# Optimization experiments

Measured on AMD Instinct MI355X. Metric: run time of the kernel, lower is better.

## Reference

```python
import jax, jax.numpy as jnp
import numpy as np

E = 512      # embed_size
H = 1024     # hidden_size
HH = H // 2  # per-direction encoder hidden
VS = 32000   # src vocab
VT = 32000   # tgt vocab
B = 32
S = 48       # src len
T = 48       # tgt decode steps (tgt_tokens has T+1 tokens incl <s>, </s>)


def setup_inputs() -> dict:
    key = jax.random.key(0)
    ks = jax.random.split(key, 24)
    rn = lambda k, shape: (jax.random.normal(k, shape) * 0.05).astype(jnp.float32)

    src_lengths = jax.random.randint(ks[0], (B,), S // 2, S + 1)
    src_tokens = jax.random.randint(ks[1], (B, S), 3, VS)
    src_tokens = jnp.where(jnp.arange(S)[None, :] < src_lengths[:, None], src_tokens, 0)
    tgt_lengths = jax.random.randint(ks[2], (B,), T // 2, T + 1)
    tgt_tokens = jax.random.randint(ks[3], (B, T + 1), 3, VT)
    tgt_tokens = jnp.where(jnp.arange(T + 1)[None, :] <= tgt_lengths[:, None], tgt_tokens, 0)

    return dict(
        enc_embed=rn(ks[4], (VS, E)),
        dec_embed=rn(ks[5], (VT, E)),
        enc_Wih_f=rn(ks[6], (4 * HH, E)), enc_Whh_f=rn(ks[7], (4 * HH, HH)),
        enc_bih_f=rn(ks[8], (4 * HH,)),   enc_bhh_f=rn(ks[9], (4 * HH,)),
        enc_Wih_b=rn(ks[10], (4 * HH, E)), enc_Whh_b=rn(ks[11], (4 * HH, HH)),
        enc_bih_b=rn(ks[12], (4 * HH,)),   enc_bhh_b=rn(ks[13], (4 * HH,)),
        dec_Wih=rn(ks[14], (4 * H, E + H)), dec_Whh=rn(ks[15], (4 * H, H)),
        dec_bih=rn(ks[16], (4 * H,)),       dec_bhh=rn(ks[17], (4 * H,)),
        Ws_W=rn(ks[18], (VT, 2 * H)), Ws_b=rn(ks[19], (VT,)),
        src_tokens=src_tokens, src_lengths=src_lengths, tgt_tokens=tgt_tokens,
    )


def _lstm_cell(x, h, c, Wih, Whh, bih, bhh):
    # torch gate order: i, f, g, o
    gates = x @ Wih.T + bih + h @ Whh.T + bhh
    i, f, g, o = jnp.split(gates, 4, axis=-1)
    c_new = jax.nn.sigmoid(f) * c + jax.nn.sigmoid(i) * jnp.tanh(g)
    h_new = jax.nn.sigmoid(o) * jnp.tanh(c_new)
    return h_new, c_new


def _masked_lstm(x, mask, Wih, Whh, bih, bhh, hid):
    # x: [B,S,Din], mask: [B,S] bool. Emulates packed LSTM: state frozen and
    # output zero at padded steps.
    Bn = x.shape[0]
    h0 = jnp.zeros((Bn, hid), x.dtype)
    c0 = jnp.zeros((Bn, hid), x.dtype)

    def step(carry, inp):
        h, c = carry
        xt, mt = inp  # [B,Din], [B]
        hn, cn = _lstm_cell(xt, h, c, Wih, Whh, bih, bhh)
        m = mt[:, None]
        h = jnp.where(m, hn, h)
        c = jnp.where(m, cn, c)
        return (h, c), h * m

    (hT, cT), outs = jax.lax.scan(step, (h0, c0), (jnp.swapaxes(x, 0, 1), mask.T))
    return jnp.swapaxes(outs, 0, 1), hT, cT  # [B,S,hid]


def reference(enc_embed, dec_embed,
              enc_Wih_f, enc_Whh_f, enc_bih_f, enc_bhh_f,
              enc_Wih_b, enc_Whh_b, enc_bih_b, enc_bhh_b,
              dec_Wih, dec_Whh, dec_bih, dec_bhh,
              Ws_W, Ws_b,
              src_tokens, src_lengths, tgt_tokens):
    src_mask = jnp.arange(S)[None, :] < src_lengths[:, None]  # [B,S]

    # ---- encoder (bi-LSTM over packed sequence) ----
    emb = enc_embed[src_tokens]  # [B,S,E]
    out_f, hf, _ = _masked_lstm(emb, src_mask, enc_Wih_f, enc_Whh_f, enc_bih_f, enc_bhh_f, HH)
    # backward direction: reverse each sequence within its own length
    rev_idx = jnp.clip(src_lengths[:, None] - 1 - jnp.arange(S)[None, :], 0)  # [B,S]
    emb_rev = jnp.take_along_axis(emb, rev_idx[:, :, None], axis=1)
    out_r, hb, _ = _masked_lstm(emb_rev, src_mask, enc_Wih_b, enc_Whh_b, enc_bih_b, enc_bhh_b, HH)
    out_b = jnp.take_along_axis(out_r, rev_idx[:, :, None], axis=1) * src_mask[:, :, None]
    src_enc = jnp.concatenate([out_f, out_b], axis=-1)  # [B,S,H]
    h0 = jnp.concatenate([hf, hb], axis=-1)  # [B,H]  (h.transpose(0,1).reshape)
    c0 = jnp.zeros_like(h0)
    # NOTE: the torch code reshapes the final LSTM c state the same way; replicate:
    # we need final c from both directions
    # (recompute via _masked_lstm returning c)
    _, _, cf = _masked_lstm(emb, src_mask, enc_Wih_f, enc_Whh_f, enc_bih_f, enc_bhh_f, HH)
    _, _, cb = _masked_lstm(emb_rev, src_mask, enc_Wih_b, enc_Whh_b, enc_bih_b, enc_bhh_b, HH)
    c0 = jnp.concatenate([cf, cb], axis=-1)

    # ---- decoder: per-step LSTM + bmm attention ----
    tgt_in = tgt_tokens[:, :-1]   # [B,T]
    target = tgt_tokens[:, 1:]    # [B,T]
    dec_emb = dec_embed[tgt_in]   # [B,T,E]
    fmask = src_mask.astype(src_enc.dtype)

    def dstep(carry, emb_t):
        h, c, wa = carry  # wa: previous attention context [B,H]
        x = jnp.concatenate([wa, emb_t], axis=-1)  # cat((context, embed)) as in torch
        h, c = _lstm_cell(x, h, c, dec_Wih, dec_Whh, dec_bih, dec_bhh)
        align = jnp.einsum('bsh,bh->bs', src_enc, h)          # bmm scores
        a = jax.nn.softmax(align, axis=1) * fmask              # softmax then mask
        a = a / jnp.sum(a, axis=1, keepdims=True)              # renormalize
        wa = jnp.einsum('bsh,bs->bh', src_enc, a)              # weighted average
        out_t = jnp.concatenate([wa, h], axis=-1)              # [B,2H]
        return (h, c, wa), out_t

    wa0 = jnp.zeros((tgt_in.shape[0], H), src_enc.dtype)
    _, outs = jax.lax.scan(dstep, (h0, c0, wa0), jnp.swapaxes(dec_emb, 0, 1))
    outs = jnp.swapaxes(outs, 0, 1)  # [B,T,2H]

    logits = jnp.einsum('btd,vd->btv', outs, Ws_W) + Ws_b
    logp = jax.nn.log_softmax(logits, axis=-1)
    nll = -jnp.take_along_axis(logp, target[:, :, None], axis=-1)[:, :, 0]
    valid = (target != 0).astype(nll.dtype)  # ignore_index=0, reduction='sum'
    return jnp.sum(nll * valid)
```

## Files before the change

kernel.cpp:

```cpp
#include <hip/hip_runtime.h>
#include <hip/hip_bf16.h>
#include <math.h>

#define EE   512
#define HJ   1024
#define VV   32000
#define BB   32
#define SS   48
#define TT   48

typedef float f32x4 __attribute__((ext_vector_type(4)));
typedef __bf16 bf16x8 __attribute__((ext_vector_type(8)));
typedef __bf16 bf16x4 __attribute__((ext_vector_type(4)));

__device__ __forceinline__ bf16x8 ld_coh_x8(const __bf16* p) {
  bf16x8 r;
  asm volatile("global_load_dwordx4 %0, %1, off sc0 sc1" : "=v"(r) : "v"(p) : "memory");
  return r;
}
__device__ __forceinline__ void st_coh_b16(__bf16* p, __bf16 v) {
  unsigned int w = __builtin_bit_cast(unsigned short, v);
  asm volatile("global_store_short %0, %1, off sc0 sc1" :: "v"(p), "v"(w) : "memory");
}

__device__ __forceinline__ void gbar(int* flags, int step, int nb) {
  asm volatile("s_waitcnt vmcnt(0)" ::: "memory");
  __syncthreads();
  if (threadIdx.x == 0)
    __hip_atomic_store(flags + blockIdx.x * 16, step, __ATOMIC_RELAXED,
                       __HIP_MEMORY_SCOPE_AGENT);
  if (threadIdx.x < nb)
    while (__hip_atomic_load(flags + threadIdx.x * 16, __ATOMIC_RELAXED,
                             __HIP_MEMORY_SCOPE_AGENT) < step)
      __builtin_amdgcn_s_sleep(1);
  __syncthreads();
}

__global__ void embed_src_kernel(const float* __restrict__ enc_embed,
                                 const int* __restrict__ src_tokens,
                                 const int* __restrict__ src_lengths,
                                 __bf16* __restrict__ emb, __bf16* __restrict__ embR) {
  int idx = blockIdx.x * 256 + threadIdx.x;
  if (idx >= BB * SS * EE) return;
  int e = idx & (EE - 1);
  int bs = idx >> 9;
  int b = bs / SS, s = bs % SS;
  int tok = src_tokens[b * SS + s];
  emb[idx] = (__bf16)enc_embed[(size_t)tok * EE + e];
  int len = src_lengths[b];
  int rs = len - 1 - s; if (rs < 0) rs = 0;
  int tokr = src_tokens[b * SS + rs];
  embR[idx] = (__bf16)enc_embed[(size_t)tokr * EE + e];
}

__global__ void embed_tgt_kernel(const float* __restrict__ dec_embed,
                                 const int* __restrict__ tgt_tokens,
                                 __bf16* __restrict__ demb) {
  int idx = blockIdx.x * 256 + threadIdx.x;
  if (idx >= BB * TT * EE) return;
  int e = idx & (EE - 1);
  int bt = idx >> 9;
  int b = bt / TT, t = bt % TT;
  int tok = tgt_tokens[b * (TT + 1) + t];
  demb[idx] = (__bf16)dec_embed[(size_t)tok * EE + e];
}

__global__ void f2bf_kernel(const float* __restrict__ src, __bf16* __restrict__ dst, int n4) {
  int i = blockIdx.x * 256 + threadIdx.x;
  if (i >= n4) return;
  float4 v = ((const float4*)src)[i];
  bf16x4 p = {(__bf16)v.x, (__bf16)v.y, (__bf16)v.z, (__bf16)v.w};
  ((bf16x4*)dst)[i] = p;
}

__global__ void f2bf_slice_kernel(const float* __restrict__ src, __bf16* __restrict__ dst,
                                  int rows, int cols, int ld, int c0) {
  int idx = blockIdx.x * 256 + threadIdx.x;
  if (idx >= rows * cols) return;
  int r = idx / cols, cc = idx % cols;
  dst[idx] = (__bf16)src[(size_t)r * ld + c0 + cc];
}

__global__ void wdec_build_kernel(const float* __restrict__ dWih, const float* __restrict__ dWhh,
                                  __bf16* __restrict__ Wd) {
  int idx = blockIdx.x * 256 + threadIdx.x;
  if (idx >= 4096 * 2048) return;
  int r = idx >> 11, k = idx & 2047;
  float v = (k < 1024) ? dWih[(size_t)r * 1536 + k] : dWhh[(size_t)r * 1024 + (k - 1024)];
  Wd[idx] = (__bf16)v;
}

__global__ void sencT_build(const __bf16* __restrict__ senc, __bf16* __restrict__ sencT) {
  int b = blockIdx.x >> 4, jt = blockIdx.x & 15;
  int j0c = jt * 64;
  __shared__ __bf16 tile[48][72];
  for (int idx = threadIdx.x; idx < 48 * 64; idx += 256) {
    int s = idx >> 6, j = idx & 63;
    tile[s][j] = senc[((size_t)b * SS + s) * 1024 + j0c + j];
  }
  __syncthreads();
  for (int idx = threadIdx.x; idx < 64 * 48; idx += 256) {
    int j = idx / 48, s = idx - j * 48;
    sencT[((size_t)b * 1024 + j0c + j) * 48 + s] = tile[s][j];
  }
}

__global__ __launch_bounds__(256) void gemm_bf16_kernel(
    const __bf16* __restrict__ A, const __bf16* __restrict__ Bm,
    const float* __restrict__ bias1, const float* __restrict__ bias2,
    float* __restrict__ C, int K, int N) {
  const int m0 = blockIdx.x * 128;
  const int n0 = blockIdx.y * 128;
  __shared__ __bf16 As[128 * 40];
  __shared__ __bf16 Bs[128 * 40];
  const int tid = threadIdx.x;
  const int lane = tid & 63, wave = tid >> 6;
  const int wm = (wave >> 1) * 64, wn = (wave & 1) * 64;
  const f32x4 zero = {0.f, 0.f, 0.f, 0.f};
  f32x4 acc[4][4];
  for (int i = 0; i < 4; i++) for (int j = 0; j < 4; j++) acc[i][j] = zero;
  const int r = tid >> 2, seg = tid & 3;
  const int mr = lane & 15, q8 = (lane >> 4) * 8;
  for (int k0 = 0; k0 < K; k0 += 32) {
    *(float4*)&As[r * 40 + seg * 8]        = *(const float4*)&A[(size_t)(m0 + r) * K + k0 + seg * 8];
    *(float4*)&As[(r + 64) * 40 + seg * 8] = *(const float4*)&A[(size_t)(m0 + r + 64) * K + k0 + seg * 8];
    *(float4*)&Bs[r * 40 + seg * 8]        = *(const float4*)&Bm[(size_t)(n0 + r) * K + k0 + seg * 8];
    *(float4*)&Bs[(r + 64) * 40 + seg * 8] = *(const float4*)&Bm[(size_t)(n0 + r + 64) * K + k0 + seg * 8];
    __syncthreads();
    bf16x8 af[4], bfr[4];
    for (int i = 0; i < 4; i++) af[i]  = *(const bf16x8*)&As[(wm + i * 16 + mr) * 40 + q8];
    for (int i = 0; i < 4; i++) bfr[i] = *(const bf16x8*)&Bs[(wn + i * 16 + mr) * 40 + q8];
    for (int i = 0; i < 4; i++)
      for (int j = 0; j < 4; j++)
        acc[i][j] = __builtin_amdgcn_mfma_f32_16x16x32_bf16(af[i], bfr[j], acc[i][j], 0, 0, 0);
    __syncthreads();
  }
  const int col = lane & 15, q = lane >> 4;
  for (int i = 0; i < 4; i++) {
    int rowg = m0 + wm + i * 16 + q * 4;
    for (int j = 0; j < 4; j++) {
      int cg = n0 + wn + j * 16 + col;
      float bb = bias1[cg] + bias2[cg];
      for (int rr = 0; rr < 4; rr++)
        C[(size_t)(rowg + rr) * N + cg] = acc[i][j][rr] + bb;
    }
  }
}

template <int BF>
__global__ __launch_bounds__(256) void logits_kernel(
    const __bf16* __restrict__ A, const void* __restrict__ Braw,
    const float* __restrict__ Wsb, float* __restrict__ rowsum) {
  const int m0 = blockIdx.x * 128;
  const int n0 = blockIdx.y * 128;
  __shared__ __bf16 As[128 * 40];
  __shared__ __bf16 Bs[128 * 40];
  const int tid = threadIdx.x;
  const int lane = tid & 63, wave = tid >> 6;
  const int wm = (wave >> 1) * 64, wn = (wave & 1) * 64;
  const f32x4 zero = {0.f, 0.f, 0.f, 0.f};
  f32x4 acc[4][4];
  for (int i = 0; i < 4; i++) for (int j = 0; j < 4; j++) acc[i][j] = zero;
  const int r = tid >> 2, seg = tid & 3;
  const int rowb = tid >> 1, koff = (tid & 1) * 16;
  const int mr = lane & 15, q8 = (lane >> 4) * 8;
  for (int k0 = 0; k0 < 2048; k0 += 32) {
    *(float4*)&As[r * 40 + seg * 8]        = *(const float4*)&A[(size_t)(m0 + r) * 2048 + k0 + seg * 8];
    *(float4*)&As[(r + 64) * 40 + seg * 8] = *(const float4*)&A[(size_t)(m0 + r + 64) * 2048 + k0 + seg * 8];
    if (BF) {
      const __bf16* Bb = (const __bf16*)Braw;
      *(float4*)&Bs[r * 40 + seg * 8]        = *(const float4*)&Bb[(size_t)(n0 + r) * 2048 + k0 + seg * 8];
      *(float4*)&Bs[(r + 64) * 40 + seg * 8] = *(const float4*)&Bb[(size_t)(n0 + r + 64) * 2048 + k0 + seg * 8];
    } else {
      const float* gb = (const float*)Braw + (size_t)(n0 + rowb) * 2048 + k0 + koff;
      float4 v0 = *(const float4*)(gb);
      float4 v1 = *(const float4*)(gb + 4);
      float4 v2 = *(const float4*)(gb + 8);
      float4 v3 = *(const float4*)(gb + 12);
      bf16x8 p0 = {(__bf16)v0.x,(__bf16)v0.y,(__bf16)v0.z,(__bf16)v0.w,
                   (__bf16)v1.x,(__bf16)v1.y,(__bf16)v1.z,(__bf16)v1.w};
      bf16x8 p1 = {(__bf16)v2.x,(__bf16)v2.y,(__bf16)v2.z,(__bf16)v2.w,
                   (__bf16)v3.x,(__bf16)v3.y,(__bf16)v3.z,(__bf16)v3.w};
      *(bf16x8*)&Bs[rowb * 40 + koff]     = p0;
      *(bf16x8*)&Bs[rowb * 40 + koff + 8] = p1;
    }
    __syncthreads();
    bf16x8 af[4], bfr[4];
    for (int i = 0; i < 4; i++) af[i]  = *(const bf16x8*)&As[(wm + i * 16 + mr) * 40 + q8];
    for (int i = 0; i < 4; i++) bfr[i] = *(const bf16x8*)&Bs[(wn + i * 16 + mr) * 40 + q8];
    for (int i = 0; i < 4; i++)
      for (int j = 0; j < 4; j++)
        acc[i][j] = __builtin_amdgcn_mfma_f32_16x16x32_bf16(af[i], bfr[j], acc[i][j], 0, 0, 0);
    __syncthreads();
  }
  const int col = lane & 15, q = lane >> 4;
  for (int i = 0; i < 4; i++) {
    float s0 = 0, s1 = 0, s2 = 0, s3 = 0;
    for (int j = 0; j < 4; j++) {
      int cg = n0 + wn + j * 16 + col;
      float bb = Wsb[cg];
      s0 += expf(acc[i][j][0] + bb);
      s1 += expf(acc[i][j][1] + bb);
      s2 += expf(acc[i][j][2] + bb);
      s3 += expf(acc[i][j][3] + bb);
    }
    for (int off = 1; off < 16; off <<= 1) {
      s0 += __shfl_xor(s0, off, 64);
      s1 += __shfl_xor(s1, off, 64);
      s2 += __shfl_xor(s2, off, 64);
      s3 += __shfl_xor(s3, off, 64);
    }
    if (col == 0) {
      int rowg = m0 + wm + i * 16 + q * 4;
      atomicAdd(&rowsum[rowg],     s0);
      atomicAdd(&rowsum[rowg + 1], s1);
      atomicAdd(&rowsum[rowg + 2], s2);
      atomicAdd(&rowsum[rowg + 3], s3);
    }
  }
}

__global__ __launch_bounds__(256) void enc_persistent(
    const __bf16* __restrict__ Wenc,
    const float* __restrict__ xg,
    const int* __restrict__ lens,
    __bf16* __restrict__ g_h,
    float* __restrict__ cenc,
    __bf16* __restrict__ ob,
    int* __restrict__ flags) {
  const int bk = blockIdx.x;
  const int dir = bk >> 7;
  const int u0 = (bk & 127) * 4;
  const int tid = threadIdx.x;
  const int lane = tid & 63, wave = tid >> 6;
  __shared__ __bf16 Wl[16 * 520];
  __shared__ float gsc[4 * 512];
  __shared__ float cl[128], hloc[128];
  {
    int row = tid >> 4, t16 = tid & 15;
    int g = row >> 2, du = row & 3;
    const __bf16* src = Wenc + ((size_t)dir * 2048 + g * 512 + u0 + du) * 512;
    for (int c = t16 * 32, e = t16 * 32 + 32; c < e; c += 8)
      *(bf16x8*)&Wl[row * 520 + c] = *(const bf16x8*)&src[c];
  }
  if (tid < 128) { cl[tid] = 0.f; hloc[tid] = 0.f; }
  __syncthreads();
  __bf16* ghd = g_h + dir * 32768;
  __bf16* obd = ob + (size_t)dir * (1536 * 512);
  const float* xgd = xg + (size_t)dir * 1536 * 2048;
  const int nr = lane & 15, q8 = (lane >> 4) * 8;
  for (int t = 0; t < SS; t++) {
    const int cur = t & 1;
    const __bf16* hc = ghd + cur * 16384;
    __bf16* hnx = ghd + (cur ^ 1) * 16384;
    float xv[4];
    if (tid < 128) {
      int b = tid >> 2, du = tid & 3;
#pragma unroll
      for (int g = 0; g < 4; g++)
        xv[g] = xgd[((size_t)b * SS + t) * 2048 + g * 512 + u0 + du];
    }
    f32x4 acc0 = {0.f,0.f,0.f,0.f}, acc1 = {0.f,0.f,0.f,0.f};
    const int kb = wave * 128;
    bf16x8 a0[4], a1[4];
#pragma unroll
    for (int ks = 0; ks < 4; ks++) {
      int k0 = kb + ks * 32;
      a0[ks] = ld_coh_x8(&hc[nr * 512 + k0 + q8]);
      a1[ks] = ld_coh_x8(&hc[(nr + 16) * 512 + k0 + q8]);
    }
    asm volatile("s_waitcnt vmcnt(0)" ::: "memory");
    __builtin_amdgcn_sched_barrier(0);
#pragma unroll
    for (int ks = 0; ks < 4; ks++) {
      int k0 = kb + ks * 32;
      bf16x8 bf_ = *(const bf16x8*)&Wl[nr * 520 + k0 + q8];
      acc0 = __builtin_amdgcn_mfma_f32_16x16x32_bf16(a0[ks], bf_, acc0, 0, 0, 0);
      acc1 = __builtin_amdgcn_mfma_f32_16x16x32_bf16(a1[ks], bf_, acc1, 0, 0, 0);
    }
#pragma unroll
    for (int rg = 0; rg < 4; rg++) {
      int m = (lane >> 4) * 4 + rg;
      gsc[wave * 512 + m * 16 + nr]       = acc0[rg];
      gsc[wave * 512 + 256 + m * 16 + nr] = acc1[rg];
    }
    __syncthreads();
    if (tid < 128) {
      int b = tid >> 2, du = tid & 3;
      float gt[4];
#pragma unroll
      for (int g = 0; g < 4; g++) {
        int base = (b >> 4) * 256 + (b & 15) * 16 + g * 4 + du;
        gt[g] = xv[g] + gsc[base] + gsc[512 + base] + gsc[1024 + base] + gsc[1536 + base];
      }
      bool m_ = t < lens[b];
      float cold = cl[tid], hold = hloc[tid];
      float si = 1.f / (1.f + __expf(-gt[0])), sf = 1.f / (1.f + __expf(-gt[1]));
      float so = 1.f / (1.f + __expf(-gt[3]));
      float cn = sf * cold + si * tanhf(gt[2]);
      float hv = so * tanhf(cn);
      float cne = m_ ? cn : cold;
      float hne = m_ ? hv : hold;
      cl[tid] = cne; hloc[tid] = hne;
      st_coh_b16(&hnx[b * 512 + u0 + du], (__bf16)hne);
      obd[((size_t)b * SS + t) * 512 + u0 + du] = m_ ? (__bf16)hv : (__bf16)0.f;
    }
    gbar(flags, t + 1, 256);
  }
  if (tid < 128) {
    int b = tid >> 2, du = tid & 3;
    cenc[(size_t)dir * 16384 + b * 512 + u0 + du] = cl[tid];
  }
}

__global__ void compose_kernel(const __bf16* __restrict__ ob, const __bf16* __restrict__ g_h,
                               const float* __restrict__ cenc, const int* __restrict__ lens,
                               __bf16* __restrict__ senc, __bf16* __restrict__ g_x0,
                               float* __restrict__ cdec) {
  int idx = blockIdx.x * 256 + threadIdx.x;
  const int N1 = 1536 * 1024;
  if (idx < N1) {
    int u = idx & 1023, bs = idx >> 10, b = bs / SS, s = bs - b * SS;
    __bf16 v;
    if (u < 512) v = ob[(size_t)bs * 512 + u];
    else {
      int len = lens[b];
      if (s < len) {
        int rs = len - 1 - s;
        v = ob[(size_t)(1536 * 512) + ((size_t)b * SS + rs) * 512 + (u - 512)];
      } else v = (__bf16)0.f;
    }
    senc[idx] = v;
  } else if (idx < N1 + 32 * 2048) {
    int k = idx - N1;
    int b = k >> 11, u = k & 2047;
    __bf16 v = (__bf16)0.f;
    if (u >= 1024) {
      int uu = u - 1024;
      v = (uu < 512) ? g_h[b * 512 + uu] : g_h[32768 + b * 512 + (uu - 512)];
    }
    g_x0[k] = v;
  } else if (idx < N1 + 32 * 2048 + 32 * 1024) {
    int k = idx - N1 - 32 * 2048;
    int b = k >> 10, u = k & 1023;
    cdec[k] = (u < 512) ? cenc[b * 512 + u] : cenc[16384 + b * 512 + (u - 512)];
  }
}

__global__ __launch_bounds__(256) void dec_persistent(
    const __bf16* __restrict__ Wd,
    const float* __restrict__ pre,
    const __bf16* __restrict__ senc,
    const __bf16* __restrict__ sencT,
    const int* __restrict__ lens,
    const float* __restrict__ cdec,
    __bf16* __restrict__ xbuf,
    __bf16* __restrict__ outs,
    int* __restrict__ flags) {
  const int bk = blockIdx.x;
  const int u0 = bk * 8;
  const int tid = threadIdx.x, lane = tid & 63, wave = tid >> 6;
  __shared__ __bf16 Wl[32 * 2056];
  __shared__ float gsc[4 * 1024];
  __shared__ float cl[256];
  __shared__ float asm_l[48];
  {
    int row = tid >> 3, t8 = tid & 7;
    int g = row >> 3, du = row & 7;
    const __bf16* src = Wd + (size_t)(g * 1024 + u0 + du) * 2048;
    for (int c = t8 * 256, e = t8 * 256 + 256; c < e; c += 8)
      *(bf16x8*)&Wl[row * 2056 + c] = *(const bf16x8*)&src[c];
  }
  cl[tid] = cdec[(size_t)(tid >> 3) * 1024 + u0 + (tid & 7)];
  __syncthreads();
  const int nr = lane & 15, q8 = (lane >> 4) * 8;
  const int bC = bk >> 2, j0 = (bk & 3) * 256;
  const int b_ = tid >> 3, du_ = tid & 7;
  float xv[4];
#pragma unroll
  for (int g = 0; g < 4; g++)
    xv[g] = pre[((size_t)b_ * TT) * 4096 + g * 1024 + u0 + du_];
  for (int t = 0; t < TT; t++) {
    const __bf16* xc = xbuf + (size_t)t * 65536;
    __bf16* xn = xbuf + (size_t)(t + 1) * 65536;
    f32x4 acc00 = {0.f,0.f,0.f,0.f}, acc01 = {0.f,0.f,0.f,0.f};
    f32x4 acc10 = {0.f,0.f,0.f,0.f}, acc11 = {0.f,0.f,0.f,0.f};
    const int kb = wave * 512;
    bf16x8 a0[16], a1[16];
    if (wave < 2) {
#pragma unroll
      for (int ks = 0; ks < 16; ks++) {
        int k0 = kb + ks * 32;
        a0[ks] = *(const bf16x8*)&xc[nr * 2048 + k0 + q8];
        a1[ks] = *(const bf16x8*)&xc[(nr + 16) * 2048 + k0 + q8];
      }
    } else {
#pragma unroll
      for (int ks = 0; ks < 16; ks++) {
        int k0 = kb + ks * 32;
        a0[ks] = ld_coh_x8(&xc[nr * 2048 + k0 + q8]);
        a1[ks] = ld_coh_x8(&xc[(nr + 16) * 2048 + k0 + q8]);
      }
      asm volatile("s_waitcnt vmcnt(0)" ::: "memory");
      __builtin_amdgcn_sched_barrier(0);
    }
#pragma unroll
    for (int ks = 0; ks < 16; ks++) {
      int k0 = kb + ks * 32;
      bf16x8 b0 = *(const bf16x8*)&Wl[nr * 2056 + k0 + q8];
      bf16x8 b1 = *(const bf16x8*)&Wl[(nr + 16) * 2056 + k0 + q8];
      acc00 = __builtin_amdgcn_mfma_f32_16x16x32_bf16(a0[ks], b0, acc00, 0, 0, 0);
      acc01 = __builtin_amdgcn_mfma_f32_16x16x32_bf16(a0[ks], b1, acc01, 0, 0, 0);
      acc10 = __builtin_amdgcn_mfma_f32_16x16x32_bf16(a1[ks], b0, acc10, 0, 0, 0);
      acc11 = __builtin_amdgcn_mfma_f32_16x16x32_bf16(a1[ks], b1, acc11, 0, 0, 0);
    }
#pragma unroll
    for (int rg = 0; rg < 4; rg++) {
      int m = (lane >> 4) * 4 + rg;
      gsc[wave * 1024 + m * 32 + nr]             = acc00[rg];
      gsc[wave * 1024 + m * 32 + 16 + nr]        = acc01[rg];
      gsc[wave * 1024 + (16 + m) * 32 + nr]      = acc10[rg];
      gsc[wave * 1024 + (16 + m) * 32 + 16 + nr] = acc11[rg];
    }
    __syncthreads();
    {
      float gt[4];
#pragma unroll
      for (int g = 0; g < 4; g++) {
        int base = b_ * 32 + g * 8 + du_;
        gt[g] = xv[g] + gsc[base] + gsc[1024 + base] + gsc[2048 + base] + gsc[3072 + base];
      }
      float cold = cl[tid];
      float si = 1.f / (1.f + __expf(-gt[0])), sf = 1.f / (1.f + __expf(-gt[1]));
      float so = 1.f / (1.f + __expf(-gt[3]));
      float cn = sf * cold + si * tanhf(gt[2]);
      float hv = so * tanhf(cn);
      cl[tid] = cn;
      __bf16 hb = (__bf16)hv;
      st_coh_b16(&xn[b_ * 2048 + 1024 + u0 + du_], hb);
      outs[((size_t)b_ * TT + t) * 2048 + 1024 + u0 + du_] = hb;
    }
    if (t + 1 < TT) {
#pragma unroll
      for (int g = 0; g < 4; g++)
        xv[g] = pre[((size_t)b_ * TT + t + 1) * 4096 + g * 1024 + u0 + du_];
    }
    gbar(flags, 2 * t + 1, 128);
    {
      int len = lens[bC];
      const __bf16* hh = xn + bC * 2048 + 1024;
      bf16x8 h0 = ld_coh_x8(&hh[lane * 16]);
      bf16x8 h1 = ld_coh_x8(&hh[lane * 16 + 8]);
      asm volatile("s_waitcnt vmcnt(0)" ::: "memory");
      __builtin_amdgcn_sched_barrier(0);
      float hf[16];
#pragma unroll
      for (int i = 0; i < 8; i++) { hf[i] = (float)h0[i]; hf[8 + i] = (float)h1[i]; }
      for (int si = 0; si < 12; si++) {
        int s = wave * 12 + si;
        if (s >= len) { if (lane == 0) asm_l[s] = -1e30f; continue; }
        const __bf16* se = senc + ((size_t)bC * SS + s) * 1024;
        bf16x8 s0 = *(const bf16x8*)&se[lane * 16];
        bf16x8 s1 = *(const bf16x8*)&se[lane * 16 + 8];
        float p = 0.f;
#pragma unroll
        for (int i = 0; i < 8; i++) p += (float)s0[i] * hf[i] + (float)s1[i] * hf[8 + i];
#pragma unroll
        for (int off = 32; off > 0; off >>= 1) p += __shfl_xor(p, off, 64);
        if (lane == 0) asm_l[s] = p;
      }
      __syncthreads();
      if (wave == 0) {
        float a = (lane < SS) ? asm_l[lane] : -1e30f;
        float mx = a;
#pragma unroll
        for (int off = 32; off > 0; off >>= 1) mx = fmaxf(mx, __shfl_xor(mx, off, 64));
        float p = (lane < SS) ? __expf(a - mx) : 0.f;
        float sm = p;
#pragma unroll
        for (int off = 32; off > 0; off >>= 1) sm += __shfl_xor(sm, off, 64);
        if (lane < SS) asm_l[lane] = p / sm;
      }
      __syncthreads();
      {
        int j = j0 + tid;
        const __bf16* srow = sencT + ((size_t)bC * 1024 + j) * 48;
        bf16x8 v0 = *(const bf16x8*)&srow[0];
        bf16x8 v1 = *(const bf16x8*)&srow[8];
        bf16x8 v2 = *(const bf16x8*)&srow[16];
        bf16x8 v3 = *(const bf16x8*)&srow[24];
        bf16x8 v4 = *(const bf16x8*)&srow[32];
        bf16x8 v5 = *(const bf16x8*)&srow[40];
        float w = 0.f;
#pragma unroll
        for (int i = 0; i < 8; i++) {
          w += asm_l[i]      * (float)v0[i];
          w += asm_l[8 + i]  * (float)v1[i];
          w += asm_l[16 + i] * (float)v2[i];
          w += asm_l[24 + i] * (float)v3[i];
          w += asm_l[32 + i] * (float)v4[i];
          w += asm_l[40 + i] * (float)v5[i];
        }
        __bf16 wb = (__bf16)w;
        st_coh_b16(&xn[bC * 2048 + j], wb);
        outs[((size_t)bC * TT + t) * 2048 + j] = wb;
      }
    }
    gbar(flags, 2 * t + 2, 128);
  }
}

__global__ __launch_bounds__(256) void tgt_logit_kernel(
    const __bf16* __restrict__ outs_bf, const float* __restrict__ WsW,
    const float* __restrict__ Wsb, const int* __restrict__ tgt_tokens,
    float* __restrict__ tlogit) {
  const int r = blockIdx.x;
  const int b = r / TT, t = r % TT;
  const int tgt = tgt_tokens[b * (TT + 1) + t + 1];
  const __bf16* a = outs_bf + (size_t)r * 2048;
  const float* w = WsW + (size_t)tgt * 2048;
  const int tid = threadIdx.x;
  float p = 0;
  for (int k = tid; k < 2048; k += 256) p += (float)a[k] * w[k];
  for (int off = 32; off > 0; off >>= 1) p += __shfl_down(p, off, 64);
  __shared__ float red[4];
  if ((tid & 63) == 0) red[tid >> 6] = p;
  __syncthreads();
  if (tid == 0) tlogit[r] = red[0] + red[1] + red[2] + red[3] + Wsb[tgt];
}

__global__ void final_kernel(const float* __restrict__ rowsum, const float* __restrict__ tlogit,
                             const int* __restrict__ tgt_tokens, float* __restrict__ out) {
  const int tid = threadIdx.x;
  float s = 0;
  for (int r = tid; r < BB * TT; r += 256) {
    int b = r / TT, t = r % TT;
    int tgt = tgt_tokens[b * (TT + 1) + t + 1];
    if (tgt != 0) s += logf(rowsum[r]) - tlogit[r];
  }
  for (int off = 32; off > 0; off >>= 1) s += __shfl_down(s, off, 64);
  __shared__ float red[4];
  if ((tid & 63) == 0) red[tid >> 6] = s;
  __syncthreads();
  if (tid == 0) out[0] = red[0] + red[1] + red[2] + red[3];
}

extern "C" void kernel_launch(void* const* d_in, const int* in_sizes, int n_in,
                              void* d_out, int out_size, void* d_ws, size_t ws_size,
                              hipStream_t stream) {
  const float* enc_embed = (const float*)d_in[0];
  const float* dec_embed = (const float*)d_in[1];
  const float* eWih_f = (const float*)d_in[2];
  const float* eWhh_f = (const float*)d_in[3];
  const float* ebih_f = (const float*)d_in[4];
  const float* ebhh_f = (const float*)d_in[5];
  const float* eWih_b = (const float*)d_in[6];
  const float* eWhh_b = (const float*)d_in[7];
  const float* ebih_b = (const float*)d_in[8];
  const float* ebhh_b = (const float*)d_in[9];
  const float* dWih = (const float*)d_in[10];
  const float* dWhh = (const float*)d_in[11];
  const float* dbih = (const float*)d_in[12];
  const float* dbhh = (const float*)d_in[13];
  const float* WsW  = (const float*)d_in[14];
  const float* Wsb  = (const float*)d_in[15];
  const int* src_tokens  = (const int*)d_in[16];
  const int* src_lengths = (const int*)d_in[17];
  const int* tgt_tokens  = (const int*)d_in[18];
  float* W = (float*)d_ws;

  size_t o = 0;
  auto alloc = [&](size_t n) { size_t r = o; o += (n + 63) & ~(size_t)63; return r; };
  const size_t flagsE = alloc(256 * 16);
  const size_t flagsD = alloc(256 * 16);
  const size_t ghenc = alloc(32768);
  const size_t rsum  = alloc(BB * TT);
  const size_t zbytes = o * sizeof(float);
  const size_t cenc  = alloc(2 * BB * 512);
  const size_t cdec  = alloc(BB * 1024);
  const size_t tlog  = alloc(BB * TT);
  const size_t xg    = alloc((size_t)2 * 1536 * 2048);
  const size_t pre   = alloc((size_t)1536 * 4096);
  const size_t obuf  = alloc((size_t)2 * 1536 * 512 / 2);
  const size_t senc  = alloc((size_t)1536 * 1024 / 2);
  const size_t sencT = alloc((size_t)32 * 1024 * 48 / 2);
  const size_t gx    = alloc((size_t)49 * 32 * 2048 / 2);
  const size_t wdec  = alloc((size_t)4096 * 2048 / 2);
  const size_t wenc  = alloc((size_t)2 * 2048 * 512 / 2);
  const size_t embbf = alloc(786432 / 2);
  const size_t embRbf= alloc(786432 / 2);
  const size_t dembbf= alloc(786432 / 2);
  const size_t wihfbf= alloc(1048576 / 2);
  const size_t wihbbf= alloc(1048576 / 2);
  const size_t dwihebf = alloc((size_t)4096 * 512 / 2);
  const size_t outsbf  = alloc((size_t)1536 * 2048 / 2);
  const size_t wsbf    = alloc((size_t)VV * 2048 / 2);
  const bool wsbf_fit  = (o * sizeof(float)) <= ws_size;

  (void)hipMemsetAsync(W, 0, zbytes, stream);

  embed_src_kernel<<<3072, 256, 0, stream>>>(enc_embed, src_tokens, src_lengths,
                                             (__bf16*)(W + embbf), (__bf16*)(W + embRbf));
  embed_tgt_kernel<<<3072, 256, 0, stream>>>(dec_embed, tgt_tokens, (__bf16*)(W + dembbf));
  f2bf_kernel<<<1024, 256, 0, stream>>>(eWih_f, (__bf16*)(W + wihfbf), 262144);
  f2bf_kernel<<<1024, 256, 0, stream>>>(eWih_b, (__bf16*)(W + wihbbf), 262144);
  f2bf_kernel<<<1024, 256, 0, stream>>>(eWhh_f, (__bf16*)(W + wenc), 262144);
  f2bf_kernel<<<1024, 256, 0, stream>>>(eWhh_b, (__bf16*)(W + wenc) + 1048576, 262144);
  f2bf_slice_kernel<<<8192, 256, 0, stream>>>(dWih, (__bf16*)(W + dwihebf), 4096, 512, 1536, 1024);
  wdec_build_kernel<<<32768, 256, 0, stream>>>(dWih, dWhh, (__bf16*)(W + wdec));
  if (wsbf_fit)
    f2bf_kernel<<<64000, 256, 0, stream>>>(WsW, (__bf16*)(W + wsbf), VV * 2048 / 4);

  gemm_bf16_kernel<<<dim3(12, 16), 256, 0, stream>>>((__bf16*)(W + embbf), (__bf16*)(W + wihfbf),
                                                     ebih_f, ebhh_f, W + xg, 512, 2048);
  gemm_bf16_kernel<<<dim3(12, 16), 256, 0, stream>>>((__bf16*)(W + embRbf), (__bf16*)(W + wihbbf),
                                                     ebih_b, ebhh_b, W + xg + (size_t)1536 * 2048, 512, 2048);
  gemm_bf16_kernel<<<dim3(12, 32), 256, 0, stream>>>((__bf16*)(W + dembbf), (__bf16*)(W + dwihebf),
                                                     dbih, dbhh, W + pre, 512, 4096);

  enc_persistent<<<256, 256, 0, stream>>>((__bf16*)(W + wenc), W + xg, src_lengths,
                                          (__bf16*)(W + ghenc), W + cenc,
                                          (__bf16*)(W + obuf), (int*)(W + flagsE));
  compose_kernel<<<6528, 256, 0, stream>>>((__bf16*)(W + obuf), (__bf16*)(W + ghenc),
                                           W + cenc, src_lengths,
                                           (__bf16*)(W + senc), (__bf16*)(W + gx), W + cdec);
  sencT_build<<<512, 256, 0, stream>>>((const __bf16*)(W + senc), (__bf16*)(W + sencT));
  dec_persistent<<<128, 256, 0, stream>>>((__bf16*)(W + wdec), W + pre, (__bf16*)(W + senc),
                                          (const __bf16*)(W + sencT),
                                          src_lengths, W + cdec, (__bf16*)(W + gx),
                                          (__bf16*)(W + outsbf), (int*)(W + flagsD));

  if (wsbf_fit)
    logits_kernel<1><<<dim3(12, 250), 256, 0, stream>>>((const __bf16*)(W + outsbf),
                                                        (const void*)(W + wsbf), Wsb, W + rsum);
  else
    logits_kernel<0><<<dim3(12, 250), 256, 0, stream>>>((const __bf16*)(W + outsbf),
                                                        (const void*)WsW, Wsb, W + rsum);
  tgt_logit_kernel<<<1536, 256, 0, stream>>>((const __bf16*)(W + outsbf), WsW, Wsb, tgt_tokens, W + tlog);
  final_kernel<<<1, 256, 0, stream>>>(W + rsum, W + tlog, tgt_tokens, (float*)d_out);
}
```

Measured before the change: 1.877 ms.

## Use direct global-to-LDS loads in logits GEMM and hoist recurrent-loop loads

In the bf16 path of the logits GEMM, tile loads now use global_load_lds to copy global memory straight into LDS. This drops the register round-trip and the padded stride. The encoder loop prefetches the next step's input gates before the barrier and caches the sequence lengths. The decoder attention loads all 12 score rows up front and interleaves their shuffle reductions so memory latency overlaps, and the barrier now takes an explicit slot index. The unpadded LDS layout may add bank conflicts, and the fetch-then-sync scheme depends on the LDS DMA completing before __syncthreads.

```diff
diff --git a/kernel.cpp b/kernel.cpp
--- a/kernel.cpp
+++ b/kernel.cpp
@@ -23,13 +23,19 @@
   asm volatile("global_store_short %0, %1, off sc0 sc1" :: "v"(p), "v"(w) : "memory");
 }
 
-__device__ __forceinline__ void gbar(int* flags, int step, int nb) {
+__device__ __forceinline__ void glds16(const __bf16* g, __bf16* l) {
+  __builtin_amdgcn_global_load_lds(
+      (const __attribute__((address_space(1))) unsigned int*)g,
+      (__attribute__((address_space(3))) unsigned int*)l, 16, 0, 0);
+}
+
+__device__ __forceinline__ void gbar(int* flags, int step, int nb, int slot) {
   asm volatile("s_waitcnt vmcnt(0)" ::: "memory");
   __syncthreads();
   if (threadIdx.x == 0)
-    __hip_atomic_store(flags + blockIdx.x * 16, step, __ATOMIC_RELAXED,
+    __hip_atomic_store(flags + slot * 16, step, __ATOMIC_RELAXED,
                        __HIP_MEMORY_SCOPE_AGENT);
-  if (threadIdx.x < nb)
+  if ((int)threadIdx.x < nb)
     while (__hip_atomic_load(flags + threadIdx.x * 16, __ATOMIC_RELAXED,
                              __HIP_MEMORY_SCOPE_AGENT) < step)
       __builtin_amdgcn_s_sleep(1);
@@ -161,17 +167,39 @@
   const f32x4 zero = {0.f, 0.f, 0.f, 0.f};
   f32x4 acc[4][4];
   for (int i = 0; i < 4; i++) for (int j = 0; j < 4; j++) acc[i][j] = zero;
-  const int r = tid >> 2, seg = tid & 3;
-  const int rowb = tid >> 1, koff = (tid & 1) * 16;
   const int mr = lane & 15, q8 = (lane >> 4) * 8;
-  for (int k0 = 0; k0 < 2048; k0 += 32) {
-    *(float4*)&As[r * 40 + seg * 8]        = *(const float4*)&A[(size_t)(m0 + r) * 2048 + k0 + seg * 8];
-    *(float4*)&As[(r + 64) * 40 + seg * 8] = *(const float4*)&A[(size_t)(m0 + r + 64) * 2048 + k0 + seg * 8];
-    if (BF) {
-      const __bf16* Bb = (const __bf16*)Braw;
-      *(float4*)&Bs[r * 40 + seg * 8]        = *(const float4*)&Bb[(size_t)(n0 + r) * 2048 + k0 + seg * 8];
-      *(float4*)&Bs[(r + 64) * 40 + seg * 8] = *(const float4*)&Bb[(size_t)(n0 + r + 64) * 2048 + k0 + seg * 8];
-    } else {
+  if (BF) {
+    const __bf16* Bb = (const __bf16*)Braw;
+    const int srow = lane >> 2, scol = (lane & 3) * 8;
+    const int wrow = wave * 32;
+    const __bf16* gA0 = A  + (size_t)(m0 + wrow + srow) * 2048 + scol;
+    const __bf16* gA1 = A  + (size_t)(m0 + wrow + 16 + srow) * 2048 + scol;
+    const __bf16* gB0 = Bb + (size_t)(n0 + wrow + srow) * 2048 + scol;
+    const __bf16* gB1 = Bb + (size_t)(n0 + wrow + 16 + srow) * 2048 + scol;
+    __bf16* lA0 = &As[wrow * 32];
+    __bf16* lA1 = &As[(wrow + 16) * 32];
+    __bf16* lB0 = &Bs[wrow * 32];
+    __bf16* lB1 = &Bs[(wrow + 16) * 32];
+    for (int k0 = 0; k0 < 2048; k0 += 32) {
+      glds16(gA0 + k0, lA0);
+      glds16(gA1 + k0, lA1);
+      glds16(gB0 + k0, lB0);
+      glds16(gB1 + k0, lB1);
+      __syncthreads();
+      bf16x8 af[4], bfr[4];
+      for (int i = 0; i < 4; i++) af[i]  = *(const bf16x8*)&As[(wm + i * 16 + mr) * 32 + q8];
+      for (int i = 0; i < 4; i++) bfr[i] = *(const bf16x8*)&Bs[(wn + i * 16 + mr) * 32 + q8];
+      for (int i = 0; i < 4; i++)
+        for (int j = 0; j < 4; j++)
+          acc[i][j] = __builtin_amdgcn_mfma_f32_16x16x32_bf16(af[i], bfr[j], acc[i][j], 0, 0, 0);
+      __syncthreads();
+    }
+  } else {
+    const int rowb = tid >> 1, koff = (tid & 1) * 16;
+    const int r = tid >> 2, seg = tid & 3;
+    for (int k0 = 0; k0 < 2048; k0 += 32) {
+      *(float4*)&As[r * 40 + seg * 8]        = *(const float4*)&A[(size_t)(m0 + r) * 2048 + k0 + seg * 8];
+      *(float4*)&As[(r + 64) * 40 + seg * 8] = *(const float4*)&A[(size_t)(m0 + r + 64) * 2048 + k0 + seg * 8];
       const float* gb = (const float*)Braw + (size_t)(n0 + rowb) * 2048 + k0 + koff;
       float4 v0 = *(const float4*)(gb);
       float4 v1 = *(const float4*)(gb + 4);
@@ -183,15 +211,15 @@
                    (__bf16)v3.x,(__bf16)v3.y,(__bf16)v3.z,(__bf16)v3.w};
       *(bf16x8*)&Bs[rowb * 40 + koff]     = p0;
       *(bf16x8*)&Bs[rowb * 40 + koff + 8] = p1;
-    }
-    __syncthreads();
-    bf16x8 af[4], bfr[4];
-    for (int i = 0; i < 4; i++) af[i]  = *(const bf16x8*)&As[(wm + i * 16 + mr) * 40 + q8];
-    for (int i = 0; i < 4; i++) bfr[i] = *(const bf16x8*)&Bs[(wn + i * 16 + mr) * 40 + q8];
-    for (int i = 0; i < 4; i++)
-      for (int j = 0; j < 4; j++)
-        acc[i][j] = __builtin_amdgcn_mfma_f32_16x16x32_bf16(af[i], bfr[j], acc[i][j], 0, 0, 0);
-    __syncthreads();
+      __syncthreads();
+      bf16x8 af[4], bfr[4];
+      for (int i = 0; i < 4; i++) af[i]  = *(const bf16x8*)&As[(wm + i * 16 + mr) * 40 + q8];
+      for (int i = 0; i < 4; i++) bfr[i] = *(const bf16x8*)&Bs[(wn + i * 16 + mr) * 40 + q8];
+      for (int i = 0; i < 4; i++)
+        for (int j = 0; j < 4; j++)
+          acc[i][j] = __builtin_amdgcn_mfma_f32_16x16x32_bf16(af[i], bfr[j], acc[i][j], 0, 0, 0);
+      __syncthreads();
+    }
   }
   const int col = lane & 15, q = lane >> 4;
   for (int i = 0; i < 4; i++) {
@@ -249,17 +277,19 @@
   __bf16* obd = ob + (size_t)dir * (1536 * 512);
   const float* xgd = xg + (size_t)dir * 1536 * 2048;
   const int nr = lane & 15, q8 = (lane >> 4) * 8;
+  int lb = 0;
+  float xv[4];
+  if (tid < 128) {
+    int b = tid >> 2, du = tid & 3;
+    lb = lens[b];
+#pragma unroll
+    for (int g = 0; g < 4; g++)
+      xv[g] = xgd[((size_t)b * SS) * 2048 + g * 512 + u0 + du];
+  }
   for (int t = 0; t < SS; t++) {
     const int cur = t & 1;
     const __bf16* hc = ghd + cur * 16384;
     __bf16* hnx = ghd + (cur ^ 1) * 16384;
-    float xv[4];
-    if (tid < 128) {
-      int b = tid >> 2, du = tid & 3;
-#pragma unroll
-      for (int g = 0; g < 4; g++)
-        xv[g] = xgd[((size_t)b * SS + t) * 2048 + g * 512 + u0 + du];
-    }
     f32x4 acc0 = {0.f,0.f,0.f,0.f}, acc1 = {0.f,0.f,0.f,0.f};
     const int kb = wave * 128;
     bf16x8 a0[4], a1[4];
@@ -293,7 +323,7 @@
         int base = (b >> 4) * 256 + (b & 15) * 16 + g * 4 + du;
         gt[g] = xv[g] + gsc[base] + gsc[512 + base] + gsc[1024 + base] + gsc[1536 + base];
       }
-      bool m_ = t < lens[b];
+      bool m_ = t < lb;
       float cold = cl[tid], hold = hloc[tid];
       float si = 1.f / (1.f + __expf(-gt[0])), sf = 1.f / (1.f + __expf(-gt[1]));
       float so = 1.f / (1.f + __expf(-gt[3]));
@@ -304,8 +334,13 @@
       cl[tid] = cne; hloc[tid] = hne;
       st_coh_b16(&hnx[b * 512 + u0 + du], (__bf16)hne);
       obd[((size_t)b * SS + t) * 512 + u0 + du] = m_ ? (__bf16)hv : (__bf16)0.f;
-    }
-    gbar(flags, t + 1, 256);
+      if (t + 1 < SS) {
+#pragma unroll
+        for (int g = 0; g < 4; g++)
+          xv[g] = xgd[((size_t)b * SS + t + 1) * 2048 + g * 512 + u0 + du];
+      }
+    }
+    gbar(flags, t + 1, 256, bk);
   }
   if (tid < 128) {
     int b = tid >> 2, du = tid & 3;
@@ -375,6 +410,7 @@
   __syncthreads();
   const int nr = lane & 15, q8 = (lane >> 4) * 8;
   const int bC = bk >> 2, j0 = (bk & 3) * 256;
+  const int lenC = lens[bC];
   const int b_ = tid >> 3, du_ = tid & 7;
   float xv[4];
 #pragma unroll
@@ -445,9 +481,8 @@
       for (int g = 0; g < 4; g++)
         xv[g] = pre[((size_t)b_ * TT + t + 1) * 4096 + g * 1024 + u0 + du_];
     }
-    gbar(flags, 2 * t + 1, 128);
+    gbar(flags, 2 * t + 1, 128, bk);
     {
-      int len = lens[bC];
       const __bf16* hh = xn + bC * 2048 + 1024;
       bf16x8 h0 = ld_coh_x8(&hh[lane * 16]);
       bf16x8 h1 = ld_coh_x8(&hh[lane * 16 + 8]);
@@ -456,18 +491,30 @@
       float hf[16];
 #pragma unroll
       for (int i = 0; i < 8; i++) { hf[i] = (float)h0[i]; hf[8 + i] = (float)h1[i]; }
+      float ps[12];
+      const __bf16* seb = senc + (size_t)bC * SS * 1024;
+#pragma unroll
       for (int si = 0; si < 12; si++) {
         int s = wave * 12 + si;
-        if (s >= len) { if (lane == 0) asm_l[s] = -1e30f; continue; }
-        const __bf16* se = senc + ((size_t)bC * SS + s) * 1024;
+        const __bf16* se = seb + (size_t)s * 1024;
         bf16x8 s0 = *(const bf16x8*)&se[lane * 16];
         bf16x8 s1 = *(const bf16x8*)&se[lane * 16 + 8];
         float p = 0.f;
 #pragma unroll
         for (int i = 0; i < 8; i++) p += (float)s0[i] * hf[i] + (float)s1[i] * hf[8 + i];
-#pragma unroll
-        for (int off = 32; off > 0; off >>= 1) p += __shfl_xor(p, off, 64);
-        if (lane == 0) asm_l[s] = p;
+        ps[si] = p;
+      }
+#pragma unroll
+      for (int off = 32; off > 0; off >>= 1) {
+#pragma unroll
+        for (int si = 0; si < 12; si++) ps[si] += __shfl_xor(ps[si], off, 64);
+      }
+      if (lane == 0) {
+#pragma unroll
+        for (int si = 0; si < 12; si++) {
+          int s = wave * 12 + si;
+          asm_l[s] = (s < lenC) ? ps[si] : -1e30f;
+        }
       }
       __syncthreads();
       if (wave == 0) {
@@ -506,7 +553,7 @@
         outs[((size_t)bC * TT + t) * 2048 + j] = wb;
       }
     }
-    gbar(flags, 2 * t + 2, 128);
+    gbar(flags, 2 * t + 2, 128, bk);
   }
 }
 
```

New measurement: 1.598 ms. -14.9%, faster.
